# Optimization experiments

Hardware: AMD Instinct MI355X
Metric: run time of the kernel (lower is better)

The kernel has to match this reference:

```python
import jax, jax.numpy as jnp
import numpy as np


def _rgcn(x, src, dst, et, basis, comp, root, bias):
    # Basis-decomposed RGCNConv (PyG semantics): per-relation mean aggregation
    # over incoming edges + root transform + bias.
    N = x.shape[0]
    R = comp.shape[0]
    W = jnp.einsum('rb,bio->rio', comp, basis)          # [R, in, out]
    xr = jnp.einsum('ni,rio->rno', x, W)                 # [R, N, out]
    msg = xr[et, src]                                    # [E, out] gather per edge
    seg = dst * R + et                                   # (target, relation) segment id
    cnt = jax.ops.segment_sum(jnp.ones(et.shape, x.dtype), seg, num_segments=N * R)
    norm = 1.0 / jnp.maximum(cnt, 1.0)                   # mean per (dst, relation)
    msg = msg * norm[seg][:, None]
    agg = jax.ops.segment_sum(msg, dst, num_segments=N)  # scatter-add to targets
    return agg + x @ root + bias


def setup_inputs() -> dict:
    key = jax.random.key(0)
    ks = jax.random.split(key, 20)
    N, E, R, B, F, D, C, NB = 100000, 1600000, 5, 512, 4, 32, 5, 2
    s = 0.1
    inp = {
        'x': jax.random.normal(ks[0], (N, F), jnp.float32),
        'edge_index': jax.random.randint(ks[1], (2, E), 0, N, dtype=jnp.int32),
        'edge_type': jax.random.randint(ks[2], (E,), 0, R, dtype=jnp.int32),
        'start_nodes': jax.random.randint(ks[3], (B,), 0, N, dtype=jnp.int32),
        # layer 0: in=F, out=D
        'basis0': jax.random.normal(ks[4], (NB, F, D), jnp.float32) * s,
        'comp0': jax.random.normal(ks[5], (R, NB), jnp.float32) * s,
        'root0': jax.random.normal(ks[6], (F, D), jnp.float32) * s,
        'bias0': jax.random.normal(ks[7], (D,), jnp.float32) * s,
        # layers 1..3: in=out=D, stacked
        'basis': jax.random.normal(ks[8], (3, NB, D, D), jnp.float32) * s,
        'comp': jax.random.normal(ks[9], (3, R, NB), jnp.float32) * s,
        'root': jax.random.normal(ks[10], (3, D, D), jnp.float32) * s,
        'bias': jax.random.normal(ks[11], (3, D), jnp.float32) * s,
        # MLP head: sum(latent_dim)=128 -> 128 -> C
        'lin1_w': jax.random.normal(ks[12], (4 * D, 128), jnp.float32) * s,
        'lin1_b': jax.random.normal(ks[13], (128,), jnp.float32) * s,
        'lin2_w': jax.random.normal(ks[14], (128, C), jnp.float32) * s,
        'lin2_b': jax.random.normal(ks[15], (C,), jnp.float32) * s,
    }
    return inp


def reference(x, edge_index, edge_type, start_nodes, basis0, comp0, root0, bias0,
              basis, comp, root, bias, lin1_w, lin1_b, lin2_w, lin2_b):
    src, dst = edge_index[0], edge_index[1]
    h = jnp.tanh(_rgcn(x, src, dst, edge_type, basis0, comp0, root0, bias0))
    states = [h]
    for l in range(basis.shape[0]):
        h = jnp.tanh(_rgcn(h, src, dst, edge_type, basis[l], comp[l], root[l], bias[l]))
        states.append(h)
    concat = jnp.concatenate(states, axis=1)             # [N, 128]
    # Per-graph readout: the walk's degenerate n_walks=1 branch, i.e. the
    # start (user) node's concatenated state (sequential backtracking walk
    # replaced by its deterministic initialization path; eval mode, no dropout).
    acc = concat[start_nodes]                            # [B, 128]
    h1 = jax.nn.relu(acc @ lin1_w + lin1_b)
    logits = h1 @ lin2_w + lin2_b
    return jax.nn.log_softmax(logits, axis=-1)
```

## Files before the change

kernel.cpp:

```cpp
#include <hip/hip_runtime.h>
#include <cstdint>

#define N_NODES 100000
#define N_EDGES 1600000
#define R_REL   5
#define NBASIS  2
#define B_START 512
#define PART_SZ 12500
#define NBUCK   256
#define BUCK_SZ 391
#define EPB     6250
#define STAGE_CAP 7000

typedef __attribute__((ext_vector_type(8))) short short8;
typedef __attribute__((ext_vector_type(4))) float f32x4;

__device__ __forceinline__ unsigned short f2bf(float f) {
    unsigned u = __float_as_uint(f);
    unsigned r = (u + 0x7FFF + ((u >> 16) & 1)) >> 16;
    return (unsigned short)r;
}
__device__ __forceinline__ float bf2f(unsigned short u) {
    return __uint_as_float(((unsigned)u) << 16);
}


__global__ __launch_bounds__(256) void k_cntb(
    const int* __restrict__ ei, int* __restrict__ bhist) {
    __shared__ int lh[NBUCK];
    int tid = threadIdx.x;
    lh[tid] = 0;
    __syncthreads();
    int base = blockIdx.x * EPB;
    for (int j = tid; j < EPB; j += 256) {
        int dst = ei[N_EDGES + base + j];
        atomicAdd(&lh[dst / BUCK_SZ], 1);
    }
    __syncthreads();
    bhist[blockIdx.x * NBUCK + tid] = lh[tid];
}

__global__ __launch_bounds__(256) void k_colscan(
    int* __restrict__ bhist, int* __restrict__ colsum) {
    __shared__ int s[256];
    int b = blockIdx.x, i = threadIdx.x;
    int v = bhist[i * NBUCK + b];
    s[i] = v;
    __syncthreads();
    for (int o = 1; o < 256; o <<= 1) {
        int t = (i >= o) ? s[i - o] : 0;
        __syncthreads();
        s[i] += t;
        __syncthreads();
    }
    bhist[i * NBUCK + b] = s[i] - v;
    if (i == 255) colsum[b] = s[255];
}

__global__ __launch_bounds__(256) void k_tiny(
    const int* __restrict__ colsum, int* __restrict__ bbase) {
    __shared__ int s[256];
    int i = threadIdx.x;
    int v = colsum[i];
    s[i] = v;
    __syncthreads();
    for (int o = 1; o < 256; o <<= 1) {
        int t = (i >= o) ? s[i - o] : 0;
        __syncthreads();
        s[i] += t;
        __syncthreads();
    }
    bbase[i] = s[i] - v;
    if (i == 255) bbase[NBUCK] = s[255];
}

__global__ __launch_bounds__(256) void k_scat(
    const int* __restrict__ ei, const int* __restrict__ et,
    const int* __restrict__ bhist, const int* __restrict__ bbase,
    int* __restrict__ arena) {
    __shared__ int lc[NBUCK];
    int tid = threadIdx.x;
    lc[tid] = bhist[blockIdx.x * NBUCK + tid] + bbase[tid];
    __syncthreads();
    int base = blockIdx.x * EPB;
    for (int j = tid; j < EPB; j += 256) {
        int e   = base + j;
        int src = ei[e];
        int dst = ei[N_EDGES + e];
        int t   = et[e];
        int bk  = dst / BUCK_SZ;
        int dl  = dst - bk * BUCK_SZ;
        int pos = atomicAdd(&lc[bk], 1);
        arena[pos] = src | (t << 17) | (dl << 20);
    }
}

__global__ __launch_bounds__(256) void k_build(
    const int* __restrict__ arena, const int* __restrict__ bbase,
    int* __restrict__ off, int* __restrict__ pk_m, float* __restrict__ nv5,
    unsigned* __restrict__ degpk) {
    __shared__ int deg5[BUCK_SZ * R_REL];
    __shared__ int loff[BUCK_SZ + 1];
    __shared__ int cur5[BUCK_SZ * R_REL];
    __shared__ int stg[STAGE_CAP];
    __shared__ int tsum[256];
    int b = blockIdx.x, tid = threadIdx.x;
    int base = bbase[b], end = bbase[b + 1];
    int count = end - base;
    for (int i = tid; i < BUCK_SZ * R_REL; i += 256) deg5[i] = 0;
    __syncthreads();
    for (int i = tid; i < count; i += 256) {
        int r  = arena[base + i];
        int dl = ((unsigned)r) >> 20;
        int t  = (r >> 17) & 7;
        atomicAdd(&deg5[dl * R_REL + t], 1);
    }
    __syncthreads();
    for (int dl = tid; dl < BUCK_SZ; dl += 256) {
        loff[dl] = deg5[dl * R_REL + 0] + deg5[dl * R_REL + 1] +
                   deg5[dl * R_REL + 2] + deg5[dl * R_REL + 3] +
                   deg5[dl * R_REL + 4];
    }
    __syncthreads();
    int d0 = 2 * tid, d1 = 2 * tid + 1;
    int va = (d0 < BUCK_SZ) ? loff[d0] : 0;
    int vb = (d1 < BUCK_SZ) ? loff[d1] : 0;
    tsum[tid] = va + vb;
    __syncthreads();
    for (int o = 1; o < 256; o <<= 1) {
        int v = (tid >= o) ? tsum[tid - o] : 0;
        __syncthreads();
        tsum[tid] += v;
        __syncthreads();
    }
    int pre = tsum[tid] - (va + vb);
    if (d0 < BUCK_SZ) loff[d0] = pre;
    if (d1 < BUCK_SZ) loff[d1] = pre + va;
    __syncthreads();
    for (int dl = tid; dl < BUCK_SZ; dl += 256) {
        int nn = b * BUCK_SZ + dl;
        int run = loff[dl];
        unsigned dp = 0;
#pragma unroll
        for (int t = 0; t < R_REL; t++) {
            cur5[dl * R_REL + t] = run;
            int c = deg5[dl * R_REL + t];
            run += c;
            int cc = c > 63 ? 63 : c;
            dp |= ((unsigned)cc) << (6 * t);
        }
        if (nn < N_NODES) {
            off[nn]   = base + loff[dl];
            degpk[nn] = dp;
#pragma unroll
            for (int t = 0; t < R_REL; t++) {
                int c = deg5[dl * R_REL + t];
                nv5[nn * R_REL + t] = 1.0f / (float)(c > 0 ? c : 1);
            }
        }
    }
    if (b == NBUCK - 1 && tid == 0) off[N_NODES] = N_EDGES;
    __syncthreads();
    for (int i = tid; i < count; i += 256) {
        int r  = arena[base + i];
        int dl = ((unsigned)r) >> 20;
        int t  = (r >> 17) & 7;
        int rk = atomicAdd(&cur5[dl * R_REL + t], 1);
        if (rk < STAGE_CAP) stg[rk] = r;
    }
    __syncthreads();
    for (int i = tid; i < count; i += 256) {
        int r = stg[i < STAGE_CAP ? i : STAGE_CAP - 1];
        pk_m[base + i] = r & 0x1FFFF;
    }
}


__global__ __launch_bounds__(256) void k_wprep(
    const float* __restrict__ basis, const float* __restrict__ comp,
    const float* __restrict__ root,  const float* __restrict__ basis0,
    const float* __restrict__ comp0, const float* __restrict__ root0,
    unsigned short* __restrict__ wf, unsigned short* __restrict__ wf0) {
    __shared__ float lw[5120];
    int tid = threadIdx.x;
    int l = blockIdx.x;
    if (l < 3) {
        for (int idx = tid; idx < 5120; idx += 256) {
            int r = idx >> 10, rem = idx & 1023, i = rem >> 5, o = rem & 31;
            lw[idx] = comp[l * 10 + r * 2 + 0] * basis[l * 2048 + i * 32 + o]
                    + comp[l * 10 + r * 2 + 1] * basis[l * 2048 + 1024 + i * 32 + o];
        }
        __syncthreads();
        for (int idx = tid; idx < 12288; idx += 256) {
            int j = idx & 7, ln = (idx >> 3) & 63;
            int s = (idx >> 9) % 12, ot = idx / 6144;
            int o = ot * 16 + (ln & 15), kk = (ln >> 4) * 8 + j;
            float val;
            if (s < 10) val = lw[(s % 5) * 1024 + kk * 32 + o];
            else        val = root[l * 1024 + kk * 32 + o];
            unsigned short hi = f2bf(val);
            unsigned short ov = ((s >= 5 && s < 10) || s == 11)
                                ? f2bf(val - bf2f(hi)) : hi;
            wf[l * 12288 + idx] = ov;
        }
    } else {
        for (int idx = tid; idx < 1024; idx += 256) {
            int k = idx >> 5, o = idx & 31;
            float val = 0.f;
            if (k < 20) {
                int r = k >> 2, i = k & 3;
                val = comp0[r * 2 + 0] * basis0[i * 32 + o]
                    + comp0[r * 2 + 1] * basis0[128 + i * 32 + o];
            } else if (k < 24) val = root0[(k - 20) * 32 + o];
            lw[idx] = val;
        }
        __syncthreads();
        for (int idx = tid; idx < 2048; idx += 256) {
            int j = idx & 7, ln = (idx >> 3) & 63;
            int s = (idx >> 9) & 1, ot = idx >> 10;
            int o = ot * 16 + (ln & 15), kk = (ln >> 4) * 8 + j;
            float val = lw[kk * 32 + o];
            unsigned short hi = f2bf(val);
            wf0[idx] = s ? f2bf(val - bf2f(hi)) : hi;
        }
    }
}


__global__ __launch_bounds__(256) void k_cvt0(
    const float* __restrict__ x, unsigned short* __restrict__ hb0,
    unsigned short* __restrict__ a0) {
    int n = blockIdx.x * 256 + threadIdx.x;
    if (n >= N_NODES) return;
    float4 xv = *(const float4*)(x + (size_t)n * 4);
    unsigned short h0 = f2bf(xv.x), h1 = f2bf(xv.y), h2 = f2bf(xv.z), h3 = f2bf(xv.w);
    unsigned short l0 = f2bf(xv.x - bf2f(h0)), l1 = f2bf(xv.y - bf2f(h1));
    unsigned short l2 = f2bf(xv.z - bf2f(h2)), l3 = f2bf(xv.w - bf2f(h3));
    unsigned long long ph = (unsigned long long)h0 | ((unsigned long long)h1 << 16)
                          | ((unsigned long long)h2 << 32) | ((unsigned long long)h3 << 48);
    unsigned long long pl = (unsigned long long)l0 | ((unsigned long long)l1 << 16)
                          | ((unsigned long long)l2 << 32) | ((unsigned long long)l3 << 48);
    *(unsigned long long*)(hb0 + (size_t)n * 4) = ph;
    unsigned short* ar = a0 + (size_t)n * 64;
    uint4 z = {0u, 0u, 0u, 0u};
    *(unsigned long long*)(ar + 20) = ph;
    *(uint4*)(ar + 24) = z;
    *(unsigned long long*)(ar + 52) = pl;
    *(uint4*)(ar + 56) = z;
}


template <int IN, int SLOTS, int AROW, int LOOFF>
__global__ __launch_bounds__(256) void k_gath(
    const unsigned short* __restrict__ hb, const int* __restrict__ pk_m,
    const float* __restrict__ nv5, const unsigned* __restrict__ degpk,
    const int* __restrict__ off, unsigned short* __restrict__ agg) {
    int tid  = threadIdx.x;
    int lane = tid & 31;
    int sub  = tid >> 5;
    int part  = blockIdx.x & 7;
    int local = (blockIdx.x >> 3) * 8 + sub;
    if (local >= PART_SZ) return;
    int n = part * PART_SZ + local;
    int c = lane % IN;
    int s = lane / IN;

    int e0 = off[n];
    unsigned dp = degpk[n];
    int chunkbase = e0;
    int mreg = (chunkbase + lane < N_EDGES) ? pk_m[chunkbase + lane] : 0;
    int e = e0;
#pragma unroll
    for (int r = 0; r < R_REL; r++) {
        int cnt = (int)((dp >> (6 * r)) & 63u);
        float acc = 0.f;
        if (SLOTS == 1) {
            for (int kb = 0; kb < cnt; kb += 4) {
                if (e + kb + 3 >= chunkbase + 32) {
                    chunkbase = e + kb;
                    mreg = (chunkbase + lane < N_EDGES) ? pk_m[chunkbase + lane] : 0;
                }
#pragma unroll
                for (int q = 0; q < 4; q++) {
                    int kq = kb + q;
                    int mq = __shfl(mreg, e + kq - chunkbase, 32);
                    unsigned short u = hb[(size_t)mq * IN + c];
                    float v = bf2f(u);
                    acc += (kq < cnt) ? v : 0.f;
                }
            }
        } else {
            for (int kb = 0; kb < cnt; kb += SLOTS) {
                if (e + kb + SLOTS - 1 >= chunkbase + 32) {
                    chunkbase = e + kb;
                    mreg = (chunkbase + lane < N_EDGES) ? pk_m[chunkbase + lane] : 0;
                }
                int kq = kb + s;
                int mq = __shfl(mreg, e + kq - chunkbase, 32);
                unsigned short u = hb[(size_t)mq * IN + c];
                float v = bf2f(u);
                acc += (kq < cnt) ? v : 0.f;
            }
        }
        e += cnt;
        if (SLOTS > 1) {
            acc += __shfl_xor(acc, 4, 32);
            acc += __shfl_xor(acc, 8, 32);
            acc += __shfl_xor(acc, 16, 32);
        }
        float sc = acc * nv5[n * R_REL + r];
        unsigned short hi = f2bf(sc);
        unsigned short lo = f2bf(sc - bf2f(hi));
        if (s == 0) {
            agg[(size_t)n * AROW + r * IN + c] = hi;
            agg[(size_t)n * AROW + LOOFF + r * IN + c] = lo;
        }
    }
}


__global__ __launch_bounds__(256) void k_gemm(
    const unsigned short* __restrict__ agg, const unsigned short* __restrict__ hbin,
    const unsigned short* __restrict__ wfl, const float* __restrict__ biasL,
    float* __restrict__ h, unsigned short* __restrict__ hbout) {
    int tid = threadIdx.x;
    int wid = tid >> 6, lane = tid & 63;
    int tile = blockIdx.x * 4 + wid;
    if (tile >= N_NODES / 16) return;
    int n0 = tile * 16;
    int row = lane & 15, kg = lane >> 4;
    const short8* ar = (const short8*)(agg + (size_t)(n0 + row) * 320 + kg * 8);
    const short8* wv = (const short8*)wfl;
    short8 hbf = *(const short8*)(hbin + (size_t)(n0 + row) * 32 + kg * 8);
    f32x4 c0 = {0.f, 0.f, 0.f, 0.f}, c1 = {0.f, 0.f, 0.f, 0.f};
#pragma unroll
    for (int s = 0; s < 5; s++) {
        short8 a = ar[s * 4];
        c0 = __builtin_amdgcn_mfma_f32_16x16x32_bf16(a, wv[s * 64 + lane], c0, 0, 0, 0);
        c1 = __builtin_amdgcn_mfma_f32_16x16x32_bf16(a, wv[(12 + s) * 64 + lane], c1, 0, 0, 0);
        c0 = __builtin_amdgcn_mfma_f32_16x16x32_bf16(a, wv[(5 + s) * 64 + lane], c0, 0, 0, 0);
        c1 = __builtin_amdgcn_mfma_f32_16x16x32_bf16(a, wv[(17 + s) * 64 + lane], c1, 0, 0, 0);
        short8 al = ar[20 + s * 4];
        c0 = __builtin_amdgcn_mfma_f32_16x16x32_bf16(al, wv[s * 64 + lane], c0, 0, 0, 0);
        c1 = __builtin_amdgcn_mfma_f32_16x16x32_bf16(al, wv[(12 + s) * 64 + lane], c1, 0, 0, 0);
    }
    c0 = __builtin_amdgcn_mfma_f32_16x16x32_bf16(hbf, wv[10 * 64 + lane], c0, 0, 0, 0);
    c1 = __builtin_amdgcn_mfma_f32_16x16x32_bf16(hbf, wv[22 * 64 + lane], c1, 0, 0, 0);
    c0 = __builtin_amdgcn_mfma_f32_16x16x32_bf16(hbf, wv[11 * 64 + lane], c0, 0, 0, 0);
    c1 = __builtin_amdgcn_mfma_f32_16x16x32_bf16(hbf, wv[23 * 64 + lane], c1, 0, 0, 0);
    float b0 = biasL[row], b1 = biasL[16 + row];
#pragma unroll
    for (int i = 0; i < 4; i++) {
        int n = n0 + kg * 4 + i;
        float t0 = tanhf(c0[i] + b0);
        float t1 = tanhf(c1[i] + b1);
        h[(size_t)n * 32 + row]      = t0;
        h[(size_t)n * 32 + 16 + row] = t1;
        hbout[(size_t)n * 32 + row]      = f2bf(t0);
        hbout[(size_t)n * 32 + 16 + row] = f2bf(t1);
    }
}

__global__ __launch_bounds__(256) void k_gemm0(
    const unsigned short* __restrict__ a0, const unsigned short* __restrict__ wf0,
    const float* __restrict__ biasL, float* __restrict__ h,
    unsigned short* __restrict__ hbout) {
    int tid = threadIdx.x;
    int wid = tid >> 6, lane = tid & 63;
    int tile = blockIdx.x * 4 + wid;
    if (tile >= N_NODES / 16) return;
    int n0 = tile * 16;
    int row = lane & 15, kg = lane >> 4;
    const short8* ar = (const short8*)(a0 + (size_t)(n0 + row) * 64 + kg * 8);
    const short8* wv = (const short8*)wf0;
    short8 a01 = ar[0], a23 = ar[4];
    f32x4 c0 = {0.f, 0.f, 0.f, 0.f}, c1 = {0.f, 0.f, 0.f, 0.f};
    c0 = __builtin_amdgcn_mfma_f32_16x16x32_bf16(a01, wv[0 * 64 + lane], c0, 0, 0, 0);
    c1 = __builtin_amdgcn_mfma_f32_16x16x32_bf16(a01, wv[2 * 64 + lane], c1, 0, 0, 0);
    c0 = __builtin_amdgcn_mfma_f32_16x16x32_bf16(a01, wv[1 * 64 + lane], c0, 0, 0, 0);
    c1 = __builtin_amdgcn_mfma_f32_16x16x32_bf16(a01, wv[3 * 64 + lane], c1, 0, 0, 0);
    c0 = __builtin_amdgcn_mfma_f32_16x16x32_bf16(a23, wv[0 * 64 + lane], c0, 0, 0, 0);
    c1 = __builtin_amdgcn_mfma_f32_16x16x32_bf16(a23, wv[2 * 64 + lane], c1, 0, 0, 0);
    float b0 = biasL[row], b1 = biasL[16 + row];
#pragma unroll
    for (int i = 0; i < 4; i++) {
        int n = n0 + kg * 4 + i;
        float t0 = tanhf(c0[i] + b0);
        float t1 = tanhf(c1[i] + b1);
        h[(size_t)n * 32 + row]      = t0;
        h[(size_t)n * 32 + 16 + row] = t1;
        hbout[(size_t)n * 32 + row]      = f2bf(t0);
        hbout[(size_t)n * 32 + 16 + row] = f2bf(t1);
    }
}


__global__ void k_save(const float* __restrict__ h, const int* __restrict__ start,
                       float* __restrict__ sav) {
    int t = blockIdx.x * blockDim.x + threadIdx.x;
    if (t < B_START * 32) {
        int b = t >> 5, ln = t & 31;
        sav[t] = h[(size_t)start[b] * 32 + ln];
    }
}

__global__ __launch_bounds__(128) void k_mlp(
    const float* __restrict__ sav, const float* __restrict__ w1,
    const float* __restrict__ b1, const float* __restrict__ w2,
    const float* __restrict__ b2, float* __restrict__ out) {
    __shared__ float cvec[128];
    __shared__ float hb[128];
    __shared__ float lg[8];
    int b = blockIdx.x, t = threadIdx.x;
    cvec[t] = sav[(t >> 5) * (B_START * 32) + b * 32 + (t & 31)];
    __syncthreads();
    float a = b1[t];
#pragma unroll 8
    for (int k = 0; k < 128; k++) a += cvec[k] * w1[k * 128 + t];
    hb[t] = fmaxf(a, 0.f);
    __syncthreads();
    if (t < 5) {
        float a2 = b2[t];
        for (int k = 0; k < 128; k++) a2 += hb[k] * w2[k * 5 + t];
        lg[t] = a2;
    }
    __syncthreads();
    if (t < 5) {
        float m = lg[0];
        for (int j = 1; j < 5; j++) m = fmaxf(m, lg[j]);
        float s = 0.f;
        for (int j = 0; j < 5; j++) s += expf(lg[j] - m);
        out[b * 5 + t] = lg[t] - m - logf(s);
    }
}


extern "C" void kernel_launch(void* const* d_in, const int* in_sizes, int n_in,
                              void* d_out, int out_size, void* d_ws, size_t ws_size,
                              hipStream_t stream) {
    const float* x      = (const float*)d_in[0];
    const int*   ei     = (const int*)d_in[1];
    const int*   etype  = (const int*)d_in[2];
    const int*   start  = (const int*)d_in[3];
    const float* basis0 = (const float*)d_in[4];
    const float* comp0  = (const float*)d_in[5];
    const float* root0  = (const float*)d_in[6];
    const float* bias0  = (const float*)d_in[7];
    const float* basis  = (const float*)d_in[8];
    const float* comp   = (const float*)d_in[9];
    const float* root   = (const float*)d_in[10];
    const float* bias   = (const float*)d_in[11];
    const float* w1     = (const float*)d_in[12];
    const float* b1     = (const float*)d_in[13];
    const float* w2     = (const float*)d_in[14];
    const float* b2     = (const float*)d_in[15];
    float* out = (float*)d_out;

    char* p = (char*)d_ws;
    auto alloc = [&](size_t bytes) -> void* {
        void* r = (void*)p;
        p += (bytes + 255) & ~(size_t)255;
        return r;
    };
    int*            bhist  = (int*)alloc((size_t)NBUCK * NBUCK * 4);
    int*            colsum = (int*)alloc(NBUCK * 4);
    int*            bbase  = (int*)alloc((NBUCK + 1) * 4);
    int*            arena  = (int*)alloc((size_t)N_EDGES * 4);
    int*            off    = (int*)alloc((N_NODES + 1) * 4);
    int*            pk_m   = (int*)alloc((size_t)N_EDGES * 4);
    float*          nv5    = (float*)alloc((size_t)N_NODES * R_REL * 4);
    unsigned*       degpk  = (unsigned*)alloc((size_t)N_NODES * 4);
    float*          h      = (float*)alloc((size_t)N_NODES * 32 * 4);
    unsigned short* hbuf   = (unsigned short*)alloc((size_t)N_NODES * 32 * 2);
    unsigned short* hb0    = (unsigned short*)alloc((size_t)N_NODES * 4 * 2);
    unsigned short* agg    = (unsigned short*)alloc((size_t)N_NODES * 320 * 2);
    unsigned short* wf     = (unsigned short*)alloc((size_t)3 * 12288 * 2);
    unsigned short* wf0    = (unsigned short*)alloc((size_t)2048 * 2);
    float*          sav    = (float*)alloc(4 * B_START * 32 * 4);

    k_cntb<<<NBUCK, 256, 0, stream>>>(ei, bhist);
    k_colscan<<<NBUCK, 256, 0, stream>>>(bhist, colsum);
    k_tiny<<<1, 256, 0, stream>>>(colsum, bbase);
    k_scat<<<NBUCK, 256, 0, stream>>>(ei, etype, bhist, bbase, arena);
    k_build<<<NBUCK, 256, 0, stream>>>(arena, bbase, off, pk_m, nv5, degpk);
    k_wprep<<<4, 256, 0, stream>>>(basis, comp, root, basis0, comp0, root0, wf, wf0);
    k_cvt0<<<(N_NODES + 255) / 256, 256, 0, stream>>>(x, hb0, agg);

    int nbGath = 8 * ((PART_SZ + 7) / 8);
    int nbGemm = (N_NODES / 16 + 3) / 4;

    k_gath<4, 8, 64, 32><<<nbGath, 256, 0, stream>>>(hb0, pk_m, nv5, degpk, off, agg);
    k_gemm0<<<nbGemm, 256, 0, stream>>>(agg, wf0, bias0, h, hbuf);
    k_save<<<64, 256, 0, stream>>>(h, start, sav);
    for (int l = 0; l < 3; l++) {
        k_gath<32, 1, 320, 160><<<nbGath, 256, 0, stream>>>(hbuf, pk_m, nv5, degpk, off, agg);
        k_gemm<<<nbGemm, 256, 0, stream>>>(agg, hbuf, wf + (size_t)l * 12288,
                                           bias + l * 32, h, hbuf);
        k_save<<<64, 256, 0, stream>>>(h, start, sav + (l + 1) * 16384);
    }

    k_mlp<<<B_START, 128, 0, stream>>>(sav, w1, b1, w2, b2, out);
}
```

Baseline: 417.8 us.

## Fuse per-layer gather aggregation with MFMA transform through shared memory

```diff
diff --git a/kernel.cpp b/kernel.cpp
--- a/kernel.cpp
+++ b/kernel.cpp
@@ -6,11 +6,11 @@
 #define R_REL   5
 #define NBASIS  2
 #define B_START 512
-#define PART_SZ 12500
 #define NBUCK   256
 #define BUCK_SZ 391
 #define EPB     6250
 #define STAGE_CAP 7000
+#define NBLK    1563
 
 typedef __attribute__((ext_vector_type(8))) short short8;
 typedef __attribute__((ext_vector_type(4))) float f32x4;
@@ -228,119 +228,95 @@
 
 
 __global__ __launch_bounds__(256) void k_cvt0(
-    const float* __restrict__ x, unsigned short* __restrict__ hb0,
-    unsigned short* __restrict__ a0) {
+    const float* __restrict__ x, unsigned short* __restrict__ hb0) {
     int n = blockIdx.x * 256 + threadIdx.x;
     if (n >= N_NODES) return;
     float4 xv = *(const float4*)(x + (size_t)n * 4);
     unsigned short h0 = f2bf(xv.x), h1 = f2bf(xv.y), h2 = f2bf(xv.z), h3 = f2bf(xv.w);
-    unsigned short l0 = f2bf(xv.x - bf2f(h0)), l1 = f2bf(xv.y - bf2f(h1));
-    unsigned short l2 = f2bf(xv.z - bf2f(h2)), l3 = f2bf(xv.w - bf2f(h3));
     unsigned long long ph = (unsigned long long)h0 | ((unsigned long long)h1 << 16)
                           | ((unsigned long long)h2 << 32) | ((unsigned long long)h3 << 48);
-    unsigned long long pl = (unsigned long long)l0 | ((unsigned long long)l1 << 16)
-                          | ((unsigned long long)l2 << 32) | ((unsigned long long)l3 << 48);
     *(unsigned long long*)(hb0 + (size_t)n * 4) = ph;
-    unsigned short* ar = a0 + (size_t)n * 64;
-    uint4 z = {0u, 0u, 0u, 0u};
-    *(unsigned long long*)(ar + 20) = ph;
-    *(uint4*)(ar + 24) = z;
-    *(unsigned long long*)(ar + 52) = pl;
-    *(uint4*)(ar + 56) = z;
-}
-
-
-template <int IN, int SLOTS, int AROW, int LOOFF>
-__global__ __launch_bounds__(256) void k_gath(
+}
+
+
+__global__ __launch_bounds__(256) void k_layer(
     const unsigned short* __restrict__ hb, const int* __restrict__ pk_m,
     const float* __restrict__ nv5, const unsigned* __restrict__ degpk,
-    const int* __restrict__ off, unsigned short* __restrict__ agg) {
-    int tid  = threadIdx.x;
-    int lane = tid & 31;
-    int sub  = tid >> 5;
-    int part  = blockIdx.x & 7;
-    int local = (blockIdx.x >> 3) * 8 + sub;
-    if (local >= PART_SZ) return;
-    int n = part * PART_SZ + local;
-    int c = lane % IN;
-    int s = lane / IN;
-
-    int e0 = off[n];
-    unsigned dp = degpk[n];
-    int chunkbase = e0;
-    int mreg = (chunkbase + lane < N_EDGES) ? pk_m[chunkbase + lane] : 0;
-    int e = e0;
-#pragma unroll
-    for (int r = 0; r < R_REL; r++) {
-        int cnt = (int)((dp >> (6 * r)) & 63u);
-        float acc = 0.f;
-        if (SLOTS == 1) {
+    const int* __restrict__ off, const unsigned short* __restrict__ wfl,
+    const float* __restrict__ biasL, float* __restrict__ h,
+    unsigned short* __restrict__ hbout) {
+    __shared__ unsigned short At[64 * 328];
+    int tid = threadIdx.x;
+    int lane32 = tid & 31;
+    int g = tid >> 5;
+    int cpos = lane32 & 7;
+    int slot = lane32 >> 3;
+    const uint2* __restrict__ hb2 = (const uint2*)hb;
+
+    for (int i = 0; i < 8; i++) {
+        int nl = g * 8 + i;
+        int n = blockIdx.x * 64 + nl;
+        int e0 = 0;
+        unsigned dp = 0;
+        if (n < N_NODES) { e0 = off[n]; dp = degpk[n]; }
+        int chunkbase = e0;
+        int mreg = (chunkbase + lane32 < N_EDGES) ? pk_m[chunkbase + lane32] : 0;
+        int e = e0;
+#pragma unroll
+        for (int r = 0; r < R_REL; r++) {
+            int cnt = (int)((dp >> (6 * r)) & 63u);
+            float nv = (n < N_NODES) ? nv5[n * R_REL + r] : 0.f;
+            float a0 = 0.f, a1 = 0.f, a2 = 0.f, a3 = 0.f;
             for (int kb = 0; kb < cnt; kb += 4) {
                 if (e + kb + 3 >= chunkbase + 32) {
                     chunkbase = e + kb;
-                    mreg = (chunkbase + lane < N_EDGES) ? pk_m[chunkbase + lane] : 0;
+                    mreg = (chunkbase + lane32 < N_EDGES) ? pk_m[chunkbase + lane32] : 0;
                 }
-#pragma unroll
-                for (int q = 0; q < 4; q++) {
-                    int kq = kb + q;
-                    int mq = __shfl(mreg, e + kq - chunkbase, 32);
-                    unsigned short u = hb[(size_t)mq * IN + c];
-                    float v = bf2f(u);
-                    acc += (kq < cnt) ? v : 0.f;
-                }
+                int kq = kb + slot;
+                int mq = __shfl(mreg, e + kq - chunkbase, 32);
+                uint2 u = hb2[(size_t)mq * 8 + cpos];
+                float msk = (kq < cnt) ? nv : 0.f;
+                a0 += msk * __uint_as_float(u.x << 16);
+                a1 += msk * __uint_as_float(u.x & 0xFFFF0000u);
+                a2 += msk * __uint_as_float(u.y << 16);
+                a3 += msk * __uint_as_float(u.y & 0xFFFF0000u);
             }
-        } else {
-            for (int kb = 0; kb < cnt; kb += SLOTS) {
-                if (e + kb + SLOTS - 1 >= chunkbase + 32) {
-                    chunkbase = e + kb;
-                    mreg = (chunkbase + lane < N_EDGES) ? pk_m[chunkbase + lane] : 0;
-                }
-                int kq = kb + s;
-                int mq = __shfl(mreg, e + kq - chunkbase, 32);
-                unsigned short u = hb[(size_t)mq * IN + c];
-                float v = bf2f(u);
-                acc += (kq < cnt) ? v : 0.f;
+            e += cnt;
+            a0 += __shfl_xor(a0, 8, 32);  a0 += __shfl_xor(a0, 16, 32);
+            a1 += __shfl_xor(a1, 8, 32);  a1 += __shfl_xor(a1, 16, 32);
+            a2 += __shfl_xor(a2, 8, 32);  a2 += __shfl_xor(a2, 16, 32);
+            a3 += __shfl_xor(a3, 8, 32);  a3 += __shfl_xor(a3, 16, 32);
+            if (slot == 0) {
+                unsigned short h0 = f2bf(a0), h1 = f2bf(a1), h2 = f2bf(a2), h3 = f2bf(a3);
+                unsigned short l0 = f2bf(a0 - bf2f(h0)), l1 = f2bf(a1 - bf2f(h1));
+                unsigned short l2 = f2bf(a2 - bf2f(h2)), l3 = f2bf(a3 - bf2f(h3));
+                uint2 hv, lv;
+                hv.x = (unsigned)h0 | ((unsigned)h1 << 16);
+                hv.y = (unsigned)h2 | ((unsigned)h3 << 16);
+                lv.x = (unsigned)l0 | ((unsigned)l1 << 16);
+                lv.y = (unsigned)l2 | ((unsigned)l3 << 16);
+                *(uint2*)&At[nl * 328 + r * 32 + cpos * 4] = hv;
+                *(uint2*)&At[nl * 328 + 160 + r * 32 + cpos * 4] = lv;
             }
         }
-        e += cnt;
-        if (SLOTS > 1) {
-            acc += __shfl_xor(acc, 4, 32);
-            acc += __shfl_xor(acc, 8, 32);
-            acc += __shfl_xor(acc, 16, 32);
-        }
-        float sc = acc * nv5[n * R_REL + r];
-        unsigned short hi = f2bf(sc);
-        unsigned short lo = f2bf(sc - bf2f(hi));
-        if (s == 0) {
-            agg[(size_t)n * AROW + r * IN + c] = hi;
-            agg[(size_t)n * AROW + LOOFF + r * IN + c] = lo;
-        }
-    }
-}
-
-
-__global__ __launch_bounds__(256) void k_gemm(
-    const unsigned short* __restrict__ agg, const unsigned short* __restrict__ hbin,
-    const unsigned short* __restrict__ wfl, const float* __restrict__ biasL,
-    float* __restrict__ h, unsigned short* __restrict__ hbout) {
-    int tid = threadIdx.x;
+    }
+    __syncthreads();
+
     int wid = tid >> 6, lane = tid & 63;
-    int tile = blockIdx.x * 4 + wid;
-    if (tile >= N_NODES / 16) return;
-    int n0 = tile * 16;
+    int n0 = blockIdx.x * 64 + wid * 16;
     int row = lane & 15, kg = lane >> 4;
-    const short8* ar = (const short8*)(agg + (size_t)(n0 + row) * 320 + kg * 8);
+    const short8* arl = (const short8*)&At[(wid * 16 + row) * 328 + kg * 8];
     const short8* wv = (const short8*)wfl;
-    short8 hbf = *(const short8*)(hbin + (size_t)(n0 + row) * 32 + kg * 8);
+    short8 hbf = *(const short8*)(hb + (size_t)(n0 + row) * 32 + kg * 8);
     f32x4 c0 = {0.f, 0.f, 0.f, 0.f}, c1 = {0.f, 0.f, 0.f, 0.f};
 #pragma unroll
     for (int s = 0; s < 5; s++) {
-        short8 a = ar[s * 4];
+        short8 a = arl[s * 4];
         c0 = __builtin_amdgcn_mfma_f32_16x16x32_bf16(a, wv[s * 64 + lane], c0, 0, 0, 0);
         c1 = __builtin_amdgcn_mfma_f32_16x16x32_bf16(a, wv[(12 + s) * 64 + lane], c1, 0, 0, 0);
         c0 = __builtin_amdgcn_mfma_f32_16x16x32_bf16(a, wv[(5 + s) * 64 + lane], c0, 0, 0, 0);
         c1 = __builtin_amdgcn_mfma_f32_16x16x32_bf16(a, wv[(17 + s) * 64 + lane], c1, 0, 0, 0);
-        short8 al = ar[20 + s * 4];
+        short8 al = arl[20 + s * 4];
         c0 = __builtin_amdgcn_mfma_f32_16x16x32_bf16(al, wv[s * 64 + lane], c0, 0, 0, 0);
         c1 = __builtin_amdgcn_mfma_f32_16x16x32_bf16(al, wv[(12 + s) * 64 + lane], c1, 0, 0, 0);
     }
@@ -352,28 +328,86 @@
 #pragma unroll
     for (int i = 0; i < 4; i++) {
         int n = n0 + kg * 4 + i;
-        float t0 = tanhf(c0[i] + b0);
-        float t1 = tanhf(c1[i] + b1);
-        h[(size_t)n * 32 + row]      = t0;
-        h[(size_t)n * 32 + 16 + row] = t1;
-        hbout[(size_t)n * 32 + row]      = f2bf(t0);
-        hbout[(size_t)n * 32 + 16 + row] = f2bf(t1);
-    }
-}
-
-__global__ __launch_bounds__(256) void k_gemm0(
-    const unsigned short* __restrict__ a0, const unsigned short* __restrict__ wf0,
-    const float* __restrict__ biasL, float* __restrict__ h,
-    unsigned short* __restrict__ hbout) {
+        if (n < N_NODES) {
+            float t0 = tanhf(c0[i] + b0);
+            float t1 = tanhf(c1[i] + b1);
+            h[(size_t)n * 32 + row]      = t0;
+            h[(size_t)n * 32 + 16 + row] = t1;
+            hbout[(size_t)n * 32 + row]      = f2bf(t0);
+            hbout[(size_t)n * 32 + 16 + row] = f2bf(t1);
+        }
+    }
+}
+
+
+__global__ __launch_bounds__(256) void k_layer0(
+    const unsigned short* __restrict__ hb0, const float* __restrict__ x,
+    const int* __restrict__ pk_m, const float* __restrict__ nv5,
+    const unsigned* __restrict__ degpk, const int* __restrict__ off,
+    const unsigned short* __restrict__ wf0, const float* __restrict__ biasL,
+    float* __restrict__ h, unsigned short* __restrict__ hbout) {
+    __shared__ unsigned short At[64 * 72];
     int tid = threadIdx.x;
+    int lane32 = tid & 31;
+    int g = tid >> 5;
+    int c = lane32 & 3;
+    int slot = lane32 >> 2;
+
+    for (int i = 0; i < 8; i++) {
+        int nl = g * 8 + i;
+        int n = blockIdx.x * 64 + nl;
+        int e0 = 0;
+        unsigned dp = 0;
+        if (n < N_NODES) { e0 = off[n]; dp = degpk[n]; }
+        int chunkbase = e0;
+        int mreg = (chunkbase + lane32 < N_EDGES) ? pk_m[chunkbase + lane32] : 0;
+        int e = e0;
+#pragma unroll
+        for (int r = 0; r < R_REL; r++) {
+            int cnt = (int)((dp >> (6 * r)) & 63u);
+            float nv = (n < N_NODES) ? nv5[n * R_REL + r] : 0.f;
+            float acc = 0.f;
+            for (int kb = 0; kb < cnt; kb += 8) {
+                if (e + kb + 7 >= chunkbase + 32) {
+                    chunkbase = e + kb;
+                    mreg = (chunkbase + lane32 < N_EDGES) ? pk_m[chunkbase + lane32] : 0;
+                }
+                int kq = kb + slot;
+                int mq = __shfl(mreg, e + kq - chunkbase, 32);
+                unsigned short u = hb0[(size_t)mq * 4 + c];
+                float msk = (kq < cnt) ? nv : 0.f;
+                acc += msk * bf2f(u);
+            }
+            e += cnt;
+            acc += __shfl_xor(acc, 4, 32);
+            acc += __shfl_xor(acc, 8, 32);
+            acc += __shfl_xor(acc, 16, 32);
+            if (slot == 0) {
+                unsigned short hi = f2bf(acc);
+                unsigned short lo = f2bf(acc - bf2f(hi));
+                At[nl * 72 + r * 4 + c]      = hi;
+                At[nl * 72 + 32 + r * 4 + c] = lo;
+            }
+        }
+        if (lane32 < 4) {
+            float xv = (n < N_NODES) ? x[(size_t)n * 4 + lane32] : 0.f;
+            unsigned short hi = f2bf(xv);
+            unsigned short lo = f2bf(xv - bf2f(hi));
+            At[nl * 72 + 20 + lane32] = hi;
+            At[nl * 72 + 52 + lane32] = lo;
+        } else if (lane32 < 12) {
+            At[nl * 72 + 20 + lane32] = 0;
+            At[nl * 72 + 52 + lane32] = 0;
+        }
+    }
+    __syncthreads();
+
     int wid = tid >> 6, lane = tid & 63;
-    int tile = blockIdx.x * 4 + wid;
-    if (tile >= N_NODES / 16) return;
-    int n0 = tile * 16;
+    int n0 = blockIdx.x * 64 + wid * 16;
     int row = lane & 15, kg = lane >> 4;
-    const short8* ar = (const short8*)(a0 + (size_t)(n0 + row) * 64 + kg * 8);
+    const short8* arl = (const short8*)&At[(wid * 16 + row) * 72 + kg * 8];
     const short8* wv = (const short8*)wf0;
-    short8 a01 = ar[0], a23 = ar[4];
+    short8 a01 = arl[0], a23 = arl[4];
     f32x4 c0 = {0.f, 0.f, 0.f, 0.f}, c1 = {0.f, 0.f, 0.f, 0.f};
     c0 = __builtin_amdgcn_mfma_f32_16x16x32_bf16(a01, wv[0 * 64 + lane], c0, 0, 0, 0);
     c1 = __builtin_amdgcn_mfma_f32_16x16x32_bf16(a01, wv[2 * 64 + lane], c1, 0, 0, 0);
@@ -385,12 +419,14 @@
 #pragma unroll
     for (int i = 0; i < 4; i++) {
         int n = n0 + kg * 4 + i;
-        float t0 = tanhf(c0[i] + b0);
-        float t1 = tanhf(c1[i] + b1);
-        h[(size_t)n * 32 + row]      = t0;
-        h[(size_t)n * 32 + 16 + row] = t1;
-        hbout[(size_t)n * 32 + row]      = f2bf(t0);
-        hbout[(size_t)n * 32 + 16 + row] = f2bf(t1);
+        if (n < N_NODES) {
+            float t0 = tanhf(c0[i] + b0);
+            float t1 = tanhf(c1[i] + b1);
+            h[(size_t)n * 32 + row]      = t0;
+            h[(size_t)n * 32 + 16 + row] = t1;
+            hbout[(size_t)n * 32 + row]      = f2bf(t0);
+            hbout[(size_t)n * 32 + 16 + row] = f2bf(t1);
+        }
     }
 }
 
@@ -471,9 +507,9 @@
     float*          nv5    = (float*)alloc((size_t)N_NODES * R_REL * 4);
     unsigned*       degpk  = (unsigned*)alloc((size_t)N_NODES * 4);
     float*          h      = (float*)alloc((size_t)N_NODES * 32 * 4);
-    unsigned short* hbuf   = (unsigned short*)alloc((size_t)N_NODES * 32 * 2);
+    unsigned short* hbA    = (unsigned short*)alloc((size_t)(N_NODES + 64) * 32 * 2);
+    unsigned short* hbB    = (unsigned short*)alloc((size_t)(N_NODES + 64) * 32 * 2);
     unsigned short* hb0    = (unsigned short*)alloc((size_t)N_NODES * 4 * 2);
-    unsigned short* agg    = (unsigned short*)alloc((size_t)N_NODES * 320 * 2);
     unsigned short* wf     = (unsigned short*)alloc((size_t)3 * 12288 * 2);
     unsigned short* wf0    = (unsigned short*)alloc((size_t)2048 * 2);
     float*          sav    = (float*)alloc(4 * B_START * 32 * 4);
@@ -484,19 +520,18 @@
     k_scat<<<NBUCK, 256, 0, stream>>>(ei, etype, bhist, bbase, arena);
     k_build<<<NBUCK, 256, 0, stream>>>(arena, bbase, off, pk_m, nv5, degpk);
     k_wprep<<<4, 256, 0, stream>>>(basis, comp, root, basis0, comp0, root0, wf, wf0);
-    k_cvt0<<<(N_NODES + 255) / 256, 256, 0, stream>>>(x, hb0, agg);
-
-    int nbGath = 8 * ((PART_SZ + 7) / 8);
-    int nbGemm = (N_NODES / 16 + 3) / 4;
-
-    k_gath<4, 8, 64, 32><<<nbGath, 256, 0, stream>>>(hb0, pk_m, nv5, degpk, off, agg);
-    k_gemm0<<<nbGemm, 256, 0, stream>>>(agg, wf0, bias0, h, hbuf);
+    k_cvt0<<<(N_NODES + 255) / 256, 256, 0, stream>>>(x, hb0);
+
+    k_layer0<<<NBLK, 256, 0, stream>>>(hb0, x, pk_m, nv5, degpk, off, wf0, bias0, h, hbA);
     k_save<<<64, 256, 0, stream>>>(h, start, sav);
+    unsigned short* hin = hbA;
+    unsigned short* hout = hbB;
     for (int l = 0; l < 3; l++) {
-        k_gath<32, 1, 320, 160><<<nbGath, 256, 0, stream>>>(hbuf, pk_m, nv5, degpk, off, agg);
-        k_gemm<<<nbGemm, 256, 0, stream>>>(agg, hbuf, wf + (size_t)l * 12288,
-                                           bias + l * 32, h, hbuf);
+        k_layer<<<NBLK, 256, 0, stream>>>(hin, pk_m, nv5, degpk, off,
+                                          wf + (size_t)l * 12288, bias + l * 32,
+                                          h, hout);
         k_save<<<64, 256, 0, stream>>>(h, start, sav + (l + 1) * 16384);
+        unsigned short* t = hin; hin = hout; hout = t;
     }
 
     k_mlp<<<B_START, 128, 0, stream>>>(sav, w1, b1, w2, b2, out);
```

Result: slower. 587.5 us (+40.6%).

## Switch aggregation to fp16 single-term and vectorize per-edge gathers

Applied to the files above, without the earlier changes.

```diff
diff --git a/kernel.cpp b/kernel.cpp
--- a/kernel.cpp
+++ b/kernel.cpp
@@ -14,6 +14,7 @@
 
 typedef __attribute__((ext_vector_type(8))) short short8;
 typedef __attribute__((ext_vector_type(4))) float f32x4;
+typedef _Float16 half8 __attribute__((ext_vector_type(8)));
 
 __device__ __forceinline__ unsigned short f2bf(float f) {
     unsigned u = __float_as_uint(f);
@@ -22,6 +23,10 @@
 }
 __device__ __forceinline__ float bf2f(unsigned short u) {
     return __uint_as_float(((unsigned)u) << 16);
+}
+__device__ __forceinline__ unsigned short f2h(float f) {
+    _Float16 h = (_Float16)f;
+    return __builtin_bit_cast(unsigned short, h);
 }
 
 
@@ -180,7 +185,8 @@
     const float* __restrict__ basis, const float* __restrict__ comp,
     const float* __restrict__ root,  const float* __restrict__ basis0,
     const float* __restrict__ comp0, const float* __restrict__ root0,
-    unsigned short* __restrict__ wf, unsigned short* __restrict__ wf0) {
+    unsigned short* __restrict__ wfh, unsigned short* __restrict__ wfr,
+    unsigned short* __restrict__ wf0) {
     __shared__ float lw[5120];
     int tid = threadIdx.x;
     int l = blockIdx.x;
@@ -191,17 +197,18 @@
                     + comp[l * 10 + r * 2 + 1] * basis[l * 2048 + 1024 + i * 32 + o];
         }
         __syncthreads();
-        for (int idx = tid; idx < 12288; idx += 256) {
-            int j = idx & 7, ln = (idx >> 3) & 63;
-            int s = (idx >> 9) % 12, ot = idx / 6144;
+        for (int idx = tid; idx < 5120; idx += 256) {
+            int ot = idx / 2560, rem = idx % 2560;
+            int s = rem >> 9, ln = (rem >> 3) & 63, j = idx & 7;
             int o = ot * 16 + (ln & 15), kk = (ln >> 4) * 8 + j;
-            float val;
-            if (s < 10) val = lw[(s % 5) * 1024 + kk * 32 + o];
-            else        val = root[l * 1024 + kk * 32 + o];
+            wfh[l * 5120 + idx] = f2h(lw[s * 1024 + kk * 32 + o]);
+        }
+        for (int idx = tid; idx < 2048; idx += 256) {
+            int ot = idx >> 10, s = (idx >> 9) & 1, ln = (idx >> 3) & 63, j = idx & 7;
+            int o = ot * 16 + (ln & 15), kk = (ln >> 4) * 8 + j;
+            float val = root[l * 1024 + kk * 32 + o];
             unsigned short hi = f2bf(val);
-            unsigned short ov = ((s >= 5 && s < 10) || s == 11)
-                                ? f2bf(val - bf2f(hi)) : hi;
-            wf[l * 12288 + idx] = ov;
+            wfr[l * 2048 + idx] = s ? f2bf(val - bf2f(hi)) : hi;
         }
     } else {
         for (int idx = tid; idx < 1024; idx += 256) {
@@ -215,139 +222,162 @@
             lw[idx] = val;
         }
         __syncthreads();
-        for (int idx = tid; idx < 2048; idx += 256) {
-            int j = idx & 7, ln = (idx >> 3) & 63;
-            int s = (idx >> 9) & 1, ot = idx >> 10;
+        for (int idx = tid; idx < 1024; idx += 256) {
+            int ot = idx >> 9, ln = (idx >> 3) & 63, j = idx & 7;
             int o = ot * 16 + (ln & 15), kk = (ln >> 4) * 8 + j;
-            float val = lw[kk * 32 + o];
-            unsigned short hi = f2bf(val);
-            wf0[idx] = s ? f2bf(val - bf2f(hi)) : hi;
+            wf0[idx] = f2h(lw[kk * 32 + o]);
         }
     }
 }
 
 
 __global__ __launch_bounds__(256) void k_cvt0(
-    const float* __restrict__ x, unsigned short* __restrict__ hb0,
-    unsigned short* __restrict__ a0) {
+    const float* __restrict__ x, unsigned short* __restrict__ hb0) {
     int n = blockIdx.x * 256 + threadIdx.x;
     if (n >= N_NODES) return;
     float4 xv = *(const float4*)(x + (size_t)n * 4);
     unsigned short h0 = f2bf(xv.x), h1 = f2bf(xv.y), h2 = f2bf(xv.z), h3 = f2bf(xv.w);
-    unsigned short l0 = f2bf(xv.x - bf2f(h0)), l1 = f2bf(xv.y - bf2f(h1));
-    unsigned short l2 = f2bf(xv.z - bf2f(h2)), l3 = f2bf(xv.w - bf2f(h3));
     unsigned long long ph = (unsigned long long)h0 | ((unsigned long long)h1 << 16)
                           | ((unsigned long long)h2 << 32) | ((unsigned long long)h3 << 48);
-    unsigned long long pl = (unsigned long long)l0 | ((unsigned long long)l1 << 16)
-                          | ((unsigned long long)l2 << 32) | ((unsigned long long)l3 << 48);
     *(unsigned long long*)(hb0 + (size_t)n * 4) = ph;
-    unsigned short* ar = a0 + (size_t)n * 64;
-    uint4 z = {0u, 0u, 0u, 0u};
-    *(unsigned long long*)(ar + 20) = ph;
-    *(uint4*)(ar + 24) = z;
-    *(unsigned long long*)(ar + 52) = pl;
-    *(uint4*)(ar + 56) = z;
-}
-
-
-template <int IN, int SLOTS, int AROW, int LOOFF>
-__global__ __launch_bounds__(256) void k_gath(
+}
+
+
+__global__ __launch_bounds__(256) void k_gath32(
     const unsigned short* __restrict__ hb, const int* __restrict__ pk_m,
     const float* __restrict__ nv5, const unsigned* __restrict__ degpk,
     const int* __restrict__ off, unsigned short* __restrict__ agg) {
     int tid  = threadIdx.x;
-    int lane = tid & 31;
+    int lane32 = tid & 31;
     int sub  = tid >> 5;
     int part  = blockIdx.x & 7;
     int local = (blockIdx.x >> 3) * 8 + sub;
     if (local >= PART_SZ) return;
     int n = part * PART_SZ + local;
-    int c = lane % IN;
-    int s = lane / IN;
+    int cpos = lane32 & 7;
+    int slot = lane32 >> 3;
+    const uint2* __restrict__ hb2 = (const uint2*)hb;
 
     int e0 = off[n];
     unsigned dp = degpk[n];
     int chunkbase = e0;
-    int mreg = (chunkbase + lane < N_EDGES) ? pk_m[chunkbase + lane] : 0;
+    int mreg = (chunkbase + lane32 < N_EDGES) ? pk_m[chunkbase + lane32] : 0;
     int e = e0;
 #pragma unroll
     for (int r = 0; r < R_REL; r++) {
         int cnt = (int)((dp >> (6 * r)) & 63u);
-        float acc = 0.f;
-        if (SLOTS == 1) {
-            for (int kb = 0; kb < cnt; kb += 4) {
-                if (e + kb + 3 >= chunkbase + 32) {
-                    chunkbase = e + kb;
-                    mreg = (chunkbase + lane < N_EDGES) ? pk_m[chunkbase + lane] : 0;
-                }
-#pragma unroll
-                for (int q = 0; q < 4; q++) {
-                    int kq = kb + q;
-                    int mq = __shfl(mreg, e + kq - chunkbase, 32);
-                    unsigned short u = hb[(size_t)mq * IN + c];
-                    float v = bf2f(u);
-                    acc += (kq < cnt) ? v : 0.f;
-                }
+        float nv = nv5[n * R_REL + r];
+        float a0 = 0.f, a1 = 0.f, a2 = 0.f, a3 = 0.f;
+        for (int kb = 0; kb < cnt; kb += 4) {
+            if (e + kb + 3 >= chunkbase + 32) {
+                chunkbase = e + kb;
+                mreg = (chunkbase + lane32 < N_EDGES) ? pk_m[chunkbase + lane32] : 0;
             }
-        } else {
-            for (int kb = 0; kb < cnt; kb += SLOTS) {
-                if (e + kb + SLOTS - 1 >= chunkbase + 32) {
-                    chunkbase = e + kb;
-                    mreg = (chunkbase + lane < N_EDGES) ? pk_m[chunkbase + lane] : 0;
-                }
-                int kq = kb + s;
-                int mq = __shfl(mreg, e + kq - chunkbase, 32);
-                unsigned short u = hb[(size_t)mq * IN + c];
-                float v = bf2f(u);
-                acc += (kq < cnt) ? v : 0.f;
+            int kq = kb + slot;
+            int mq = __shfl(mreg, e + kq - chunkbase, 32);
+            uint2 u = hb2[(size_t)mq * 8 + cpos];
+            float msk = (kq < cnt) ? nv : 0.f;
+            a0 += msk * __uint_as_float(u.x << 16);
+            a1 += msk * __uint_as_float(u.x & 0xFFFF0000u);
+            a2 += msk * __uint_as_float(u.y << 16);
+            a3 += msk * __uint_as_float(u.y & 0xFFFF0000u);
+        }
+        e += cnt;
+        a0 += __shfl_xor(a0, 8, 32);  a0 += __shfl_xor(a0, 16, 32);
+        a1 += __shfl_xor(a1, 8, 32);  a1 += __shfl_xor(a1, 16, 32);
+        a2 += __shfl_xor(a2, 8, 32);  a2 += __shfl_xor(a2, 16, 32);
+        a3 += __shfl_xor(a3, 8, 32);  a3 += __shfl_xor(a3, 16, 32);
+        if (slot == 0) {
+            uint2 pk;
+            pk.x = (unsigned)f2h(a0) | ((unsigned)f2h(a1) << 16);
+            pk.y = (unsigned)f2h(a2) | ((unsigned)f2h(a3) << 16);
+            *(uint2*)(agg + (size_t)n * 160 + r * 32 + cpos * 4) = pk;
+        }
+    }
+}
+
+
+__global__ __launch_bounds__(256) void k_gath0(
+    const unsigned short* __restrict__ hb0, const float* __restrict__ x,
+    const int* __restrict__ pk_m, const float* __restrict__ nv5,
+    const unsigned* __restrict__ degpk, const int* __restrict__ off,
+    unsigned short* __restrict__ a0v) {
+    int tid  = threadIdx.x;
+    int lane32 = tid & 31;
+    int sub  = tid >> 5;
+    int part  = blockIdx.x & 7;
+    int local = (blockIdx.x >> 3) * 8 + sub;
+    if (local >= PART_SZ) return;
+    int n = part * PART_SZ + local;
+    int cpos = lane32 & 1;
+    int slot = lane32 >> 1;
+    const unsigned* __restrict__ hb32 = (const unsigned*)hb0;
+
+    int e0 = off[n];
+    unsigned dp = degpk[n];
+    int chunkbase = e0;
+    int mreg = (chunkbase + lane32 < N_EDGES) ? pk_m[chunkbase + lane32] : 0;
+    int e = e0;
+#pragma unroll
+    for (int r = 0; r < R_REL; r++) {
+        int cnt = (int)((dp >> (6 * r)) & 63u);
+        float nv = nv5[n * R_REL + r];
+        float p0 = 0.f, p1 = 0.f;
+        for (int kb = 0; kb < cnt; kb += 16) {
+            if (e + kb + 15 >= chunkbase + 32) {
+                chunkbase = e + kb;
+                mreg = (chunkbase + lane32 < N_EDGES) ? pk_m[chunkbase + lane32] : 0;
             }
+            int kq = kb + slot;
+            int mq = __shfl(mreg, e + kq - chunkbase, 32);
+            unsigned u = hb32[(size_t)mq * 2 + cpos];
+            float msk = (kq < cnt) ? nv : 0.f;
+            p0 += msk * __uint_as_float(u << 16);
+            p1 += msk * __uint_as_float(u & 0xFFFF0000u);
         }
         e += cnt;
-        if (SLOTS > 1) {
-            acc += __shfl_xor(acc, 4, 32);
-            acc += __shfl_xor(acc, 8, 32);
-            acc += __shfl_xor(acc, 16, 32);
-        }
-        float sc = acc * nv5[n * R_REL + r];
-        unsigned short hi = f2bf(sc);
-        unsigned short lo = f2bf(sc - bf2f(hi));
-        if (s == 0) {
-            agg[(size_t)n * AROW + r * IN + c] = hi;
-            agg[(size_t)n * AROW + LOOFF + r * IN + c] = lo;
-        }
+        p0 += __shfl_xor(p0, 2, 32); p0 += __shfl_xor(p0, 4, 32);
+        p0 += __shfl_xor(p0, 8, 32); p0 += __shfl_xor(p0, 16, 32);
+        p1 += __shfl_xor(p1, 2, 32); p1 += __shfl_xor(p1, 4, 32);
+        p1 += __shfl_xor(p1, 8, 32); p1 += __shfl_xor(p1, 16, 32);
+        if (slot == 0) {
+            unsigned pk = (unsigned)f2h(p0) | ((unsigned)f2h(p1) << 16);
+            *(unsigned*)(a0v + (size_t)n * 32 + r * 4 + cpos * 2) = pk;
+        }
+    }
+    if (lane32 < 12) {
+        float xv = (lane32 < 4) ? x[(size_t)n * 4 + lane32] : 0.f;
+        a0v[(size_t)n * 32 + 20 + lane32] = (lane32 < 4) ? f2h(xv) : (unsigned short)0;
     }
 }
 
 
 __global__ __launch_bounds__(256) void k_gemm(
     const unsigned short* __restrict__ agg, const unsigned short* __restrict__ hbin,
-    const unsigned short* __restrict__ wfl, const float* __restrict__ biasL,
-    float* __restrict__ h, unsigned short* __restrict__ hbout) {
+    const unsigned short* __restrict__ wfhl, const unsigned short* __restrict__ wfrl,
+    const float* __restrict__ biasL, float* __restrict__ h,
+    unsigned short* __restrict__ hbout) {
     int tid = threadIdx.x;
     int wid = tid >> 6, lane = tid & 63;
     int tile = blockIdx.x * 4 + wid;
     if (tile >= N_NODES / 16) return;
     int n0 = tile * 16;
     int row = lane & 15, kg = lane >> 4;
-    const short8* ar = (const short8*)(agg + (size_t)(n0 + row) * 320 + kg * 8);
-    const short8* wv = (const short8*)wfl;
+    const half8* ar = (const half8*)(agg + (size_t)(n0 + row) * 160 + kg * 8);
+    const half8* wh = (const half8*)wfhl;
+    const short8* wr = (const short8*)wfrl;
     short8 hbf = *(const short8*)(hbin + (size_t)(n0 + row) * 32 + kg * 8);
     f32x4 c0 = {0.f, 0.f, 0.f, 0.f}, c1 = {0.f, 0.f, 0.f, 0.f};
 #pragma unroll
     for (int s = 0; s < 5; s++) {
-        short8 a = ar[s * 4];
-        c0 = __builtin_amdgcn_mfma_f32_16x16x32_bf16(a, wv[s * 64 + lane], c0, 0, 0, 0);
-        c1 = __builtin_amdgcn_mfma_f32_16x16x32_bf16(a, wv[(12 + s) * 64 + lane], c1, 0, 0, 0);
-        c0 = __builtin_amdgcn_mfma_f32_16x16x32_bf16(a, wv[(5 + s) * 64 + lane], c0, 0, 0, 0);
-        c1 = __builtin_amdgcn_mfma_f32_16x16x32_bf16(a, wv[(17 + s) * 64 + lane], c1, 0, 0, 0);
-        short8 al = ar[20 + s * 4];
-        c0 = __builtin_amdgcn_mfma_f32_16x16x32_bf16(al, wv[s * 64 + lane], c0, 0, 0, 0);
-        c1 = __builtin_amdgcn_mfma_f32_16x16x32_bf16(al, wv[(12 + s) * 64 + lane], c1, 0, 0, 0);
-    }
-    c0 = __builtin_amdgcn_mfma_f32_16x16x32_bf16(hbf, wv[10 * 64 + lane], c0, 0, 0, 0);
-    c1 = __builtin_amdgcn_mfma_f32_16x16x32_bf16(hbf, wv[22 * 64 + lane], c1, 0, 0, 0);
-    c0 = __builtin_amdgcn_mfma_f32_16x16x32_bf16(hbf, wv[11 * 64 + lane], c0, 0, 0, 0);
-    c1 = __builtin_amdgcn_mfma_f32_16x16x32_bf16(hbf, wv[23 * 64 + lane], c1, 0, 0, 0);
+        half8 a = ar[s * 4];
+        c0 = __builtin_amdgcn_mfma_f32_16x16x32_f16(a, wh[s * 64 + lane], c0, 0, 0, 0);
+        c1 = __builtin_amdgcn_mfma_f32_16x16x32_f16(a, wh[320 + s * 64 + lane], c1, 0, 0, 0);
+    }
+    c0 = __builtin_amdgcn_mfma_f32_16x16x32_bf16(hbf, wr[lane], c0, 0, 0, 0);
+    c0 = __builtin_amdgcn_mfma_f32_16x16x32_bf16(hbf, wr[64 + lane], c0, 0, 0, 0);
+    c1 = __builtin_amdgcn_mfma_f32_16x16x32_bf16(hbf, wr[128 + lane], c1, 0, 0, 0);
+    c1 = __builtin_amdgcn_mfma_f32_16x16x32_bf16(hbf, wr[192 + lane], c1, 0, 0, 0);
     float b0 = biasL[row], b1 = biasL[16 + row];
 #pragma unroll
     for (int i = 0; i < 4; i++) {
@@ -362,7 +392,7 @@
 }
 
 __global__ __launch_bounds__(256) void k_gemm0(
-    const unsigned short* __restrict__ a0, const unsigned short* __restrict__ wf0,
+    const unsigned short* __restrict__ a0v, const unsigned short* __restrict__ wf0,
     const float* __restrict__ biasL, float* __restrict__ h,
     unsigned short* __restrict__ hbout) {
     int tid = threadIdx.x;
@@ -371,16 +401,11 @@
     if (tile >= N_NODES / 16) return;
     int n0 = tile * 16;
     int row = lane & 15, kg = lane >> 4;
-    const short8* ar = (const short8*)(a0 + (size_t)(n0 + row) * 64 + kg * 8);
-    const short8* wv = (const short8*)wf0;
-    short8 a01 = ar[0], a23 = ar[4];
+    half8 a = *(const half8*)(a0v + (size_t)(n0 + row) * 32 + kg * 8);
+    const half8* wv = (const half8*)wf0;
     f32x4 c0 = {0.f, 0.f, 0.f, 0.f}, c1 = {0.f, 0.f, 0.f, 0.f};
-    c0 = __builtin_amdgcn_mfma_f32_16x16x32_bf16(a01, wv[0 * 64 + lane], c0, 0, 0, 0);
-    c1 = __builtin_amdgcn_mfma_f32_16x16x32_bf16(a01, wv[2 * 64 + lane], c1, 0, 0, 0);
-    c0 = __builtin_amdgcn_mfma_f32_16x16x32_bf16(a01, wv[1 * 64 + lane], c0, 0, 0, 0);
-    c1 = __builtin_amdgcn_mfma_f32_16x16x32_bf16(a01, wv[3 * 64 + lane], c1, 0, 0, 0);
-    c0 = __builtin_amdgcn_mfma_f32_16x16x32_bf16(a23, wv[0 * 64 + lane], c0, 0, 0, 0);
-    c1 = __builtin_amdgcn_mfma_f32_16x16x32_bf16(a23, wv[2 * 64 + lane], c1, 0, 0, 0);
+    c0 = __builtin_amdgcn_mfma_f32_16x16x32_f16(a, wv[lane], c0, 0, 0, 0);
+    c1 = __builtin_amdgcn_mfma_f32_16x16x32_f16(a, wv[64 + lane], c1, 0, 0, 0);
     float b0 = biasL[row], b1 = biasL[16 + row];
 #pragma unroll
     for (int i = 0; i < 4; i++) {
@@ -471,11 +496,13 @@
     float*          nv5    = (float*)alloc((size_t)N_NODES * R_REL * 4);
     unsigned*       degpk  = (unsigned*)alloc((size_t)N_NODES * 4);
     float*          h      = (float*)alloc((size_t)N_NODES * 32 * 4);
-    unsigned short* hbuf   = (unsigned short*)alloc((size_t)N_NODES * 32 * 2);
+    unsigned short* hbuf   = (unsigned short*)alloc((size_t)(N_NODES + 64) * 32 * 2);
     unsigned short* hb0    = (unsigned short*)alloc((size_t)N_NODES * 4 * 2);
-    unsigned short* agg    = (unsigned short*)alloc((size_t)N_NODES * 320 * 2);
-    unsigned short* wf     = (unsigned short*)alloc((size_t)3 * 12288 * 2);
-    unsigned short* wf0    = (unsigned short*)alloc((size_t)2048 * 2);
+    unsigned short* a0v    = (unsigned short*)alloc((size_t)(N_NODES + 64) * 32 * 2);
+    unsigned short* agg    = (unsigned short*)alloc((size_t)(N_NODES + 64) * 160 * 2);
+    unsigned short* wfh    = (unsigned short*)alloc((size_t)3 * 5120 * 2);
+    unsigned short* wfr    = (unsigned short*)alloc((size_t)3 * 2048 * 2);
+    unsigned short* wf0    = (unsigned short*)alloc((size_t)1024 * 2);
     float*          sav    = (float*)alloc(4 * B_START * 32 * 4);
 
     k_cntb<<<NBUCK, 256, 0, stream>>>(ei, bhist);
@@ -483,19 +510,21 @@
     k_tiny<<<1, 256, 0, stream>>>(colsum, bbase);
     k_scat<<<NBUCK, 256, 0, stream>>>(ei, etype, bhist, bbase, arena);
     k_build<<<NBUCK, 256, 0, stream>>>(arena, bbase, off, pk_m, nv5, degpk);
-    k_wprep<<<4, 256, 0, stream>>>(basis, comp, root, basis0, comp0, root0, wf, wf0);
-    k_cvt0<<<(N_NODES + 255) / 256, 256, 0, stream>>>(x, hb0, agg);
+    k_wprep<<<4, 256, 0, stream>>>(basis, comp, root, basis0, comp0, root0,
+                                   wfh, wfr, wf0);
+    k_cvt0<<<(N_NODES + 255) / 256, 256, 0, stream>>>(x, hb0);
 
     int nbGath = 8 * ((PART_SZ + 7) / 8);
     int nbGemm = (N_NODES / 16 + 3) / 4;
 
-    k_gath<4, 8, 64, 32><<<nbGath, 256, 0, stream>>>(hb0, pk_m, nv5, degpk, off, agg);
-    k_gemm0<<<nbGemm, 256, 0, stream>>>(agg, wf0, bias0, h, hbuf);
+    k_gath0<<<nbGath, 256, 0, stream>>>(hb0, x, pk_m, nv5, degpk, off, a0v);
+    k_gemm0<<<nbGemm, 256, 0, stream>>>(a0v, wf0, bias0, h, hbuf);
     k_save<<<64, 256, 0, stream>>>(h, start, sav);
     for (int l = 0; l < 3; l++) {
-        k_gath<32, 1, 320, 160><<<nbGath, 256, 0, stream>>>(hbuf, pk_m, nv5, degpk, off, agg);
-        k_gemm<<<nbGemm, 256, 0, stream>>>(agg, hbuf, wf + (size_t)l * 12288,
-                                           bias + l * 32, h, hbuf);
+        k_gath32<<<nbGath, 256, 0, stream>>>(hbuf, pk_m, nv5, degpk, off, agg);
+        k_gemm<<<nbGemm, 256, 0, stream>>>(agg, hbuf, wfh + (size_t)l * 5120,
+                                           wfr + (size_t)l * 2048, bias + l * 32,
+                                           h, hbuf);
         k_save<<<64, 256, 0, stream>>>(h, start, sav + (l + 1) * 16384);
     }
 
```

Result: faster. 380.1 us (-9.0%).
